# Kernel tuning notes

Measured on AMD Instinct MI355X. Metric: run time of the kernel, lower is better.

## Reference

```python
import jax, jax.numpy as jnp
import numpy as np

SEQ_LEN = 512
JOINT_DIM = 96
DECAY = 0.8


def _predefined_weights(n: int, decay: float) -> np.ndarray:
    # W[i, j] = decay**(i-j) for j <= i, each row normalized to sum 1.
    i = np.arange(n)[:, None]
    j = np.arange(n)[None, :]
    lower = j <= i
    exponent = np.where(lower, i - j, 0)
    w = np.where(lower, decay ** exponent.astype(np.float64), 0.0)
    row_sum = w.sum(axis=1, keepdims=True)
    w = np.where(row_sum > 0, w / row_sum, w)
    return w.astype(np.float32)


def setup_inputs() -> dict:
    key = jax.random.key(0)
    kx, ko = jax.random.split(key)
    x = jax.random.normal(kx, (64, SEQ_LEN, JOINT_DIM), dtype=jnp.float32)
    # learnable parameter (initialized to zeros in the module; small noise for generality)
    learnable_offset = 0.02 * jax.random.normal(ko, (JOINT_DIM, SEQ_LEN, SEQ_LEN), dtype=jnp.float32)
    predefined_weights = jnp.asarray(_predefined_weights(SEQ_LEN, DECAY))
    return {"x": x, "learnable_offset": learnable_offset, "predefined_weights": predefined_weights}


def reference(x, learnable_offset, predefined_weights):
    # masks[j] = softmax(predefined + offset[j], axis=-1)   -> [J, N, N]
    masks = jax.nn.softmax(predefined_weights[None, :, :] + learnable_offset, axis=-1)
    # out[b, n, j] = sum_m masks[j, n, m] * x[b, m, j]      -> [B, N, J]
    return jnp.einsum('jnm,bmj->bnj', masks, x)
```

## Files before the change

kernel.cpp:

```cpp
#include <hip/hip_runtime.h>

#define BATCH 64
#define SEQ   512
#define JDIM  96
#define TN    64
#define KC    64
#define LDB   72

typedef __attribute__((ext_vector_type(8))) short bf16x8;
typedef __attribute__((ext_vector_type(4))) float f32x4;

__device__ __forceinline__ unsigned short f2bf(float f) {
  unsigned u = __float_as_uint(f);
  u += 0x7FFFu + ((u >> 16) & 1u);
  return (unsigned short)(u >> 16);
}

__global__ __launch_bounds__(256) void transpose_in_kernel(
    const float* __restrict__ x, unsigned short* __restrict__ xT) {
  __shared__ float tile[JDIM * 65];
  const int r0 = blockIdx.x * 64;
  const int R = BATCH * SEQ;
  for (int idx = threadIdx.x; idx < 64 * JDIM; idx += 256) {
    int rr = idx / JDIM, j = idx - rr * JDIM;
    tile[j * 65 + rr] = x[(size_t)(r0 + rr) * JDIM + j];
  }
  __syncthreads();
  for (int idx = threadIdx.x; idx < JDIM * 32; idx += 256) {
    int j = idx >> 5, rg = idx & 31;
    float f0 = tile[j * 65 + 2 * rg];
    float f1 = tile[j * 65 + 2 * rg + 1];
    unsigned pk = (unsigned)f2bf(f0) | ((unsigned)f2bf(f1) << 16);
    *(unsigned*)(&xT[(size_t)j * R + r0 + 2 * rg]) = pk;
  }
}

__global__ __launch_bounds__(256, 3) void fused_kernel(
    const unsigned short* __restrict__ xT,
    const float* __restrict__ off,
    const float* __restrict__ pre,
    float* __restrict__ outT) {
  __shared__ unsigned short As[BATCH * LDB];
  __shared__ unsigned short Bs[TN * LDB];
  __shared__ float Lred[TN * 17];
  __shared__ float Linv[TN];

  const int j  = blockIdx.x % JDIM;
  const int n0 = (blockIdx.x / JDIM) * TN;

  const int tid  = threadIdx.x;
  const int lane = tid & 63;
  const int wid  = tid >> 6;
  const int ln   = lane & 15;
  const int quad = lane >> 4;
  const int bw   = (wid & 1) * 32;
  const int nw   = (wid >> 1) * 32;

  f32x4 acc[2][2];
#pragma unroll
  for (int i = 0; i < 2; ++i)
#pragma unroll
    for (int q = 0; q < 2; ++q) acc[i][q] = (f32x4){0.f, 0.f, 0.f, 0.f};
  float Lpart[4] = {0.f, 0.f, 0.f, 0.f};

  const unsigned short* xTj = xT + (size_t)j * (BATCH * SEQ);
  const float* offj = off + (size_t)j * (SEQ * SEQ);

  const int a_kg = tid & 7;
  const int a_b  = tid >> 3;
  const int b_mg = tid & 15;
  const int b_n  = tid >> 4;

  for (int ch = 0; ch < SEQ / KC; ++ch) {
    const int m0 = ch * KC;
#pragma unroll
    for (int p = 0; p < 2; ++p) {
      const int b = a_b + 32 * p;
      uint4 v = *(const uint4*)(xTj + (size_t)b * SEQ + m0 + 8 * a_kg);
      *(uint4*)(&As[b * LDB + 8 * a_kg]) = v;
    }
#pragma unroll
    for (int p = 0; p < 4; ++p) {
      const int nl = b_n + 16 * p;
      const float4 o  = *(const float4*)(offj + (size_t)(n0 + nl) * SEQ + m0 + 4 * b_mg);
      const float4 pr = *(const float4*)(pre  + (size_t)(n0 + nl) * SEQ + m0 + 4 * b_mg);
      const float e0 = __expf(o.x + pr.x);
      const float e1 = __expf(o.y + pr.y);
      const float e2 = __expf(o.z + pr.z);
      const float e3 = __expf(o.w + pr.w);
      Lpart[p] += (e0 + e1) + (e2 + e3);
      uint2 pk;
      pk.x = (unsigned)f2bf(e0) | ((unsigned)f2bf(e1) << 16);
      pk.y = (unsigned)f2bf(e2) | ((unsigned)f2bf(e3) << 16);
      *(uint2*)(&Bs[nl * LDB + 4 * b_mg]) = pk;
    }
    __syncthreads();
#pragma unroll
    for (int ks = 0; ks < KC; ks += 32) {
      bf16x8 afrag[2], bfrag[2];
#pragma unroll
      for (int i = 0; i < 2; ++i)
        afrag[i] = *(const bf16x8*)(&As[(bw + 16 * i + ln) * LDB + ks + 8 * quad]);
#pragma unroll
      for (int q = 0; q < 2; ++q)
        bfrag[q] = *(const bf16x8*)(&Bs[(nw + 16 * q + ln) * LDB + ks + 8 * quad]);
#pragma unroll
      for (int i = 0; i < 2; ++i)
#pragma unroll
        for (int q = 0; q < 2; ++q)
          acc[i][q] = __builtin_amdgcn_mfma_f32_16x16x32_bf16(afrag[i], bfrag[q], acc[i][q], 0, 0, 0);
    }
    __syncthreads();
  }

#pragma unroll
  for (int p = 0; p < 4; ++p) Lred[(b_n + 16 * p) * 17 + b_mg] = Lpart[p];
  __syncthreads();
  if (tid < TN) {
    float s = 0.f;
#pragma unroll
    for (int i = 0; i < 16; ++i) s += Lred[tid * 17 + i];
    Linv[tid] = 1.0f / s;
  }
  __syncthreads();

  float* outTj = outT + (size_t)j * (SEQ * BATCH);
#pragma unroll
  for (int q = 0; q < 2; ++q) {
    const int nc = nw + 16 * q + ln;
    const float linv = Linv[nc];
#pragma unroll
    for (int i = 0; i < 2; ++i) {
      float4 v;
      v.x = acc[i][q][0] * linv;
      v.y = acc[i][q][1] * linv;
      v.z = acc[i][q][2] * linv;
      v.w = acc[i][q][3] * linv;
      *(float4*)(&outTj[(size_t)(n0 + nc) * BATCH + bw + 16 * i + 4 * quad]) = v;
    }
  }
}

__global__ __launch_bounds__(256) void transpose_out_kernel(
    const float* __restrict__ outT, float* __restrict__ out) {
  __shared__ float tile[JDIM * 65];
  const int n = blockIdx.x;
  for (int idx = threadIdx.x; idx < JDIM * BATCH; idx += 256) {
    int j = idx >> 6, b = idx & 63;
    tile[j * 65 + b] = outT[((size_t)j * SEQ + n) * BATCH + b];
  }
  __syncthreads();
  for (int idx = threadIdx.x; idx < JDIM * BATCH; idx += 256) {
    int b = idx / JDIM, j = idx - b * JDIM;
    out[((size_t)b * SEQ + n) * JDIM + j] = tile[j * 65 + b];
  }
}

extern "C" void kernel_launch(void* const* d_in, const int* in_sizes, int n_in,
                              void* d_out, int out_size, void* d_ws, size_t ws_size,
                              hipStream_t stream) {
  const float* x   = (const float*)d_in[0];
  const float* off = (const float*)d_in[1];
  const float* pre = (const float*)d_in[2];
  float* out = (float*)d_out;

  unsigned short* xT = (unsigned short*)d_ws;
  float* outT = (float*)((char*)d_ws + (size_t)JDIM * BATCH * SEQ * sizeof(unsigned short));

  transpose_in_kernel<<<BATCH * SEQ / 64, 256, 0, stream>>>(x, xT);
  fused_kernel<<<JDIM * (SEQ / TN), 256, 0, stream>>>(xT, off, pre, outT);
  transpose_out_kernel<<<SEQ, 256, 0, stream>>>(outT, out);
}
```

Measured before the change: 178.2 us.

## Prefetch next K-chunk into registers and vectorize transpose kernels

The fused kernel now loads the next chunk's x, offset and predefined-weight data into registers right after the barrier, so those global loads overlap the MFMA work on the current chunk. The input and output transpose kernels switch to 16-byte float4/uint4 global loads and stores instead of scalar accesses. The prefetch adds live registers, which could lower occupancy under the launch bounds of 3 waves per SIMD, and the scalar LDS stores in the transposes may have some bank conflicts.

Result: slower. 183.7 us (+3.1%).

```diff
diff --git a/kernel.cpp b/kernel.cpp
--- a/kernel.cpp
+++ b/kernel.cpp
@@ -5,6 +5,7 @@
 #define JDIM  96
 #define TN    64
 #define KC    64
+#define NCH   (SEQ / KC)
 #define LDB   72
 
 typedef __attribute__((ext_vector_type(8))) short bf16x8;
@@ -21,17 +22,24 @@
   __shared__ float tile[JDIM * 65];
   const int r0 = blockIdx.x * 64;
   const int R = BATCH * SEQ;
-  for (int idx = threadIdx.x; idx < 64 * JDIM; idx += 256) {
-    int rr = idx / JDIM, j = idx - rr * JDIM;
-    tile[j * 65 + rr] = x[(size_t)(r0 + rr) * JDIM + j];
-  }
-  __syncthreads();
-  for (int idx = threadIdx.x; idx < JDIM * 32; idx += 256) {
-    int j = idx >> 5, rg = idx & 31;
-    float f0 = tile[j * 65 + 2 * rg];
-    float f1 = tile[j * 65 + 2 * rg + 1];
-    unsigned pk = (unsigned)f2bf(f0) | ((unsigned)f2bf(f1) << 16);
-    *(unsigned*)(&xT[(size_t)j * R + r0 + 2 * rg]) = pk;
+  for (int idx = threadIdx.x; idx < 64 * 24; idx += 256) {
+    int rr = idx / 24, jg = idx - rr * 24;
+    float4 v = *(const float4*)(x + (size_t)(r0 + rr) * JDIM + 4 * jg);
+    tile[(4 * jg + 0) * 65 + rr] = v.x;
+    tile[(4 * jg + 1) * 65 + rr] = v.y;
+    tile[(4 * jg + 2) * 65 + rr] = v.z;
+    tile[(4 * jg + 3) * 65 + rr] = v.w;
+  }
+  __syncthreads();
+  for (int idx = threadIdx.x; idx < JDIM * 8; idx += 256) {
+    int jj = idx >> 3, rg = idx & 7;
+    const float* t = &tile[jj * 65 + 8 * rg];
+    uint4 pk;
+    pk.x = (unsigned)f2bf(t[0]) | ((unsigned)f2bf(t[1]) << 16);
+    pk.y = (unsigned)f2bf(t[2]) | ((unsigned)f2bf(t[3]) << 16);
+    pk.z = (unsigned)f2bf(t[4]) | ((unsigned)f2bf(t[5]) << 16);
+    pk.w = (unsigned)f2bf(t[6]) | ((unsigned)f2bf(t[7]) << 16);
+    *(uint4*)(&xT[(size_t)jj * R + r0 + 8 * rg]) = pk;
   }
 }
 
@@ -71,30 +79,49 @@
   const int b_mg = tid & 15;
   const int b_n  = tid >> 4;
 
-  for (int ch = 0; ch < SEQ / KC; ++ch) {
-    const int m0 = ch * KC;
-#pragma unroll
-    for (int p = 0; p < 2; ++p) {
-      const int b = a_b + 32 * p;
-      uint4 v = *(const uint4*)(xTj + (size_t)b * SEQ + m0 + 8 * a_kg);
-      *(uint4*)(&As[b * LDB + 8 * a_kg]) = v;
-    }
+  const unsigned short* pA = xTj + (size_t)a_b * SEQ + 8 * a_kg;
+  const float* pO = offj + (size_t)(n0 + b_n) * SEQ + 4 * b_mg;
+  const float* pP = pre  + (size_t)(n0 + b_n) * SEQ + 4 * b_mg;
+
+  uint4  rA[2];
+  float4 rO[4], rP[4];
+
+  rA[0] = *(const uint4*)(pA);
+  rA[1] = *(const uint4*)(pA + 32 * SEQ);
+#pragma unroll
+  for (int p = 0; p < 4; ++p) {
+    rO[p] = *(const float4*)(pO + (size_t)(16 * p) * SEQ);
+    rP[p] = *(const float4*)(pP + (size_t)(16 * p) * SEQ);
+  }
+
+  for (int ch = 0; ch < NCH; ++ch) {
+    *(uint4*)(&As[a_b * LDB + 8 * a_kg]) = rA[0];
+    *(uint4*)(&As[(a_b + 32) * LDB + 8 * a_kg]) = rA[1];
 #pragma unroll
     for (int p = 0; p < 4; ++p) {
-      const int nl = b_n + 16 * p;
-      const float4 o  = *(const float4*)(offj + (size_t)(n0 + nl) * SEQ + m0 + 4 * b_mg);
-      const float4 pr = *(const float4*)(pre  + (size_t)(n0 + nl) * SEQ + m0 + 4 * b_mg);
-      const float e0 = __expf(o.x + pr.x);
-      const float e1 = __expf(o.y + pr.y);
-      const float e2 = __expf(o.z + pr.z);
-      const float e3 = __expf(o.w + pr.w);
+      const float e0 = __expf(rO[p].x + rP[p].x);
+      const float e1 = __expf(rO[p].y + rP[p].y);
+      const float e2 = __expf(rO[p].z + rP[p].z);
+      const float e3 = __expf(rO[p].w + rP[p].w);
       Lpart[p] += (e0 + e1) + (e2 + e3);
       uint2 pk;
       pk.x = (unsigned)f2bf(e0) | ((unsigned)f2bf(e1) << 16);
       pk.y = (unsigned)f2bf(e2) | ((unsigned)f2bf(e3) << 16);
-      *(uint2*)(&Bs[nl * LDB + 4 * b_mg]) = pk;
+      *(uint2*)(&Bs[(b_n + 16 * p) * LDB + 4 * b_mg]) = pk;
     }
     __syncthreads();
+
+    if (ch + 1 < NCH) {
+      const int m1 = (ch + 1) * KC;
+      rA[0] = *(const uint4*)(pA + m1);
+      rA[1] = *(const uint4*)(pA + 32 * SEQ + m1);
+#pragma unroll
+      for (int p = 0; p < 4; ++p) {
+        rO[p] = *(const float4*)(pO + (size_t)(16 * p) * SEQ + m1);
+        rP[p] = *(const float4*)(pP + (size_t)(16 * p) * SEQ + m1);
+      }
+    }
+
 #pragma unroll
     for (int ks = 0; ks < KC; ks += 32) {
       bf16x8 afrag[2], bfrag[2];
@@ -145,14 +172,21 @@
     const float* __restrict__ outT, float* __restrict__ out) {
   __shared__ float tile[JDIM * 65];
   const int n = blockIdx.x;
-  for (int idx = threadIdx.x; idx < JDIM * BATCH; idx += 256) {
-    int j = idx >> 6, b = idx & 63;
-    tile[j * 65 + b] = outT[((size_t)j * SEQ + n) * BATCH + b];
-  }
-  __syncthreads();
-  for (int idx = threadIdx.x; idx < JDIM * BATCH; idx += 256) {
-    int b = idx / JDIM, j = idx - b * JDIM;
-    out[((size_t)b * SEQ + n) * JDIM + j] = tile[j * 65 + b];
+  for (int idx = threadIdx.x; idx < JDIM * 16; idx += 256) {
+    int jj = idx >> 4, g = idx & 15;
+    float4 v = *(const float4*)(outT + ((size_t)jj * SEQ + n) * BATCH + 4 * g);
+    float* t = &tile[jj * 65 + 4 * g];
+    t[0] = v.x; t[1] = v.y; t[2] = v.z; t[3] = v.w;
+  }
+  __syncthreads();
+  for (int idx = threadIdx.x; idx < BATCH * 24; idx += 256) {
+    int b = idx / 24, jg = idx - b * 24;
+    float4 w;
+    w.x = tile[(4 * jg + 0) * 65 + b];
+    w.y = tile[(4 * jg + 1) * 65 + b];
+    w.z = tile[(4 * jg + 2) * 65 + b];
+    w.w = tile[(4 * jg + 3) * 65 + b];
+    *(float4*)(out + ((size_t)b * SEQ + n) * JDIM + 4 * jg) = w;
   }
 }
 
```
